# Kernel tuning notes

Measured on AMD Instinct MI355X. Metric: run time of the kernel, lower is better.

The kernel has to match this reference:

```python
import jax, jax.numpy as jnp
import numpy as np

S = 16          # spatial_size (adaptive pool output per dim)
EPS = 1e-8      # torch.cosine_similarity eps

def _avg_pool3d(x, s):
    # exact adaptive avg pool when D,H,W divisible by s
    B, C, D, H, W = x.shape
    kd, kh, kw = D // s, H // s, W // s
    x = x.reshape(B, C, s, kd, s, kh, s, kw)
    return x.mean(axis=(3, 5, 7))  # (B, C, s, s, s)

def _flatten_rows(x):
    # (B,C,s,s,s) -> (B*s^3, C), matching view+transpose+flatten
    B, C = x.shape[0], x.shape[1]
    return x.reshape(B, C, -1).transpose(0, 2, 1).reshape(-1, C)

def _cos_sim_matrix(a):
    # pairwise cosine similarity via normalize + GEMM
    norms = jnp.maximum(jnp.linalg.norm(a, axis=-1, keepdims=True), EPS)
    an = a / norms
    return an @ an.T  # (N, N)

def setup_inputs() -> dict:
    key = jax.random.key(0)
    k1, k2 = jax.random.split(key)
    shape = (2, 32, 64, 64, 64)
    p1 = jax.random.normal(k1, shape, dtype=jnp.float32)
    p2 = jax.random.normal(k2, shape, dtype=jnp.float32)
    return {"p1": p1, "p2": p2}

def reference(p1, p2):
    aa = _flatten_rows(_avg_pool3d(p1, S))  # (N, C), N = B*S^3
    bb = _flatten_rows(_avg_pool3d(p2, S))
    sim_a = _cos_sim_matrix(aa)
    sim_b = _cos_sim_matrix(bb)
    return jnp.mean((sim_a - sim_b) ** 2)  # MSELoss
```

## Files before the change

### kernel.cpp

```cpp
#include <hip/hip_runtime.h>
#include <hip/hip_bf16.h>


#define HW   4096
#define DHW  262144
#define NROW 8192
#define C    32

__global__ __launch_bounds__(256) void pool_norm_kernel(
    const float* __restrict__ p1, const float* __restrict__ p2,
    float* __restrict__ An, float* __restrict__ Bn)
{
    const int bid = blockIdx.x;
    const int y = bid & 15;
    const int z = (bid >> 4) & 15;
    const int b = bid >> 8;

    const float* __restrict__ src = (blockIdx.y == 0) ? p1 : p2;
    float* __restrict__ dst       = (blockIdx.y == 0) ? An : Bn;

    const int tid = threadIdx.x;
    const int x  = tid & 15;
    const int c0 = tid >> 4;

    __shared__ float pool[C][16];
    __shared__ float inv_norm[16];

    float pooled[2];
    #pragma unroll
    for (int cc = 0; cc < 2; ++cc) {
        const int c = c0 + cc * 16;
        const float* base = src + (size_t)(b * C + c) * DHW
                                + (4 * z) * HW + (4 * y) * 64 + 4 * x;
        float s = 0.f;
        #pragma unroll
        for (int dz = 0; dz < 4; ++dz) {
            #pragma unroll
            for (int dy = 0; dy < 4; ++dy) {
                const float4 v = *reinterpret_cast<const float4*>(base + dz * HW + dy * 64);
                s += (v.x + v.y) + (v.z + v.w);
            }
        }
        pooled[cc] = s * (1.0f / 64.0f);
        pool[c][x] = pooled[cc];
    }
    __syncthreads();

    if (tid < 16) {
        float ss = 0.f;
        #pragma unroll
        for (int c = 0; c < C; ++c) { const float v = pool[c][tid]; ss += v * v; }
        inv_norm[tid] = 1.0f / fmaxf(sqrtf(ss), 1e-8f);
    }
    __syncthreads();

    const int row = ((b * 16 + z) * 16 + y) * 16 + x;
    const float inv = inv_norm[x];
    #pragma unroll
    for (int cc = 0; cc < 2; ++cc) {
        const int c = c0 + cc * 16;
        dst[(size_t)row * C + c] = pooled[cc] * inv;
    }
}

__global__ __launch_bounds__(256) void gram_kernel(
    const float* __restrict__ An, const float* __restrict__ Bn,
    float* __restrict__ G)
{
    const int tid = threadIdx.x;
    const int k  = tid >> 3;
    const int l4 = (tid & 7) * 4;

    __shared__ float As[32 * C];
    __shared__ float Bs[32 * C];

    float gaa[4] = {0.f, 0.f, 0.f, 0.f};
    float gab[4] = {0.f, 0.f, 0.f, 0.f};
    float gbb[4] = {0.f, 0.f, 0.f, 0.f};

    const int row0 = blockIdx.x * 64;
    for (int t = 0; t < 2; ++t) {
        const int r = row0 + t * 32;
        reinterpret_cast<float4*>(As)[tid] =
            reinterpret_cast<const float4*>(An + (size_t)r * C)[tid];
        reinterpret_cast<float4*>(Bs)[tid] =
            reinterpret_cast<const float4*>(Bn + (size_t)r * C)[tid];
        __syncthreads();

        #pragma unroll
        for (int i = 0; i < 32; ++i) {
            const float a_k = As[i * C + k];
            const float b_k = Bs[i * C + k];
            const float4 a_l = *reinterpret_cast<const float4*>(&As[i * C + l4]);
            const float4 b_l = *reinterpret_cast<const float4*>(&Bs[i * C + l4]);
            gaa[0] += a_k * a_l.x;  gaa[1] += a_k * a_l.y;
            gaa[2] += a_k * a_l.z;  gaa[3] += a_k * a_l.w;
            gab[0] += a_k * b_l.x;  gab[1] += a_k * b_l.y;
            gab[2] += a_k * b_l.z;  gab[3] += a_k * b_l.w;
            gbb[0] += b_k * b_l.x;  gbb[1] += b_k * b_l.y;
            gbb[2] += b_k * b_l.z;  gbb[3] += b_k * b_l.w;
        }
        __syncthreads();
    }

    float* Gaa = G;
    float* Gab = G + 1024;
    float* Gbb = G + 2048;
    #pragma unroll
    for (int j = 0; j < 4; ++j) {
        atomicAdd(&Gaa[k * C + l4 + j], gaa[j]);
        atomicAdd(&Gab[k * C + l4 + j], gab[j]);
        atomicAdd(&Gbb[k * C + l4 + j], gbb[j]);
    }
}

__global__ __launch_bounds__(1024) void finalize_kernel(
    const float* __restrict__ G, float* __restrict__ out)
{
    const int t = threadIdx.x;
    const float gaa = G[t];
    const float gab = G[1024 + t];
    const float gbb = G[2048 + t];
    float v = gaa * gaa + gbb * gbb - 2.f * gab * gab;

    __shared__ float red[16];
    #pragma unroll
    for (int off = 32; off > 0; off >>= 1) v += __shfl_down(v, off);
    if ((t & 63) == 0) red[t >> 6] = v;
    __syncthreads();
    if (t < 16) {
        float w = red[t];
        #pragma unroll
        for (int off = 8; off > 0; off >>= 1) w += __shfl_down(w, off);
        if (t == 0) out[0] = w / ((float)NROW * (float)NROW);
    }
}

extern "C" void kernel_launch(void* const* d_in, const int* in_sizes, int n_in,
                              void* d_out, int out_size, void* d_ws, size_t ws_size,
                              hipStream_t stream) {
    const float* p1 = (const float*)d_in[0];
    const float* p2 = (const float*)d_in[1];
    float* out = (float*)d_out;

    float* An = (float*)d_ws;
    float* Bn = An + (size_t)NROW * C;
    float* G  = Bn + (size_t)NROW * C;

    hipMemsetAsync(G, 0, 3 * 1024 * sizeof(float), stream);

    dim3 g1(512, 2);
    pool_norm_kernel<<<g1, 256, 0, stream>>>(p1, p2, An, Bn);
    gram_kernel<<<128, 256, 0, stream>>>(An, Bn, G);
    finalize_kernel<<<1, 1024, 0, stream>>>(G, out);
}
```

Measured before the change: 162.6 us.

## Coalesce pooling loads across wave lanes and split gram atomics into partitions

The pooling kernel now runs 1024 threads per block. Each wave handles two channels, and its lanes cover the dy rows and x positions, so every float4 load is contiguous across lanes and all loads are issued before any summing. Partial sums are combined with wave shuffles. The gram kernel processes 32 rows per block across twice as many blocks, and it spreads its atomic adds over 8 partitioned copies of G to reduce contention; finalize then sums the partitions. The costs are a larger memset and the extra partition reads in finalize.

```diff
diff --git a/kernel.cpp b/kernel.cpp
--- a/kernel.cpp
+++ b/kernel.cpp
@@ -2,64 +2,69 @@
 #include <hip/hip_bf16.h>
 
 
-#define HW   4096
-#define DHW  262144
-#define NROW 8192
-#define C    32
+#define HW    4096
+#define DHW   262144
+#define NROW  8192
+#define C     32
+#define NPART 8
 
-__global__ __launch_bounds__(256) void pool_norm_kernel(
+__global__ __launch_bounds__(1024) void pool_norm_kernel(
     const float* __restrict__ p1, const float* __restrict__ p2,
     float* __restrict__ An, float* __restrict__ Bn)
 {
     const int bid = blockIdx.x;
-    const int y = bid & 15;
-    const int z = (bid >> 4) & 15;
-    const int b = bid >> 8;
+    const int yo = bid & 15;
+    const int zo = (bid >> 4) & 15;
+    const int b  = bid >> 8;
 
     const float* __restrict__ src = (blockIdx.y == 0) ? p1 : p2;
     float* __restrict__ dst       = (blockIdx.y == 0) ? An : Bn;
 
-    const int tid = threadIdx.x;
-    const int x  = tid & 15;
-    const int c0 = tid >> 4;
+    const int tid  = threadIdx.x;
+    const int wv   = tid >> 6;
+    const int lane = tid & 63;
+    const int dy   = lane >> 4;
+    const int x4   = lane & 15;
 
     __shared__ float pool[C][16];
     __shared__ float inv_norm[16];
 
-    float pooled[2];
+    float4 v[2][4];
     #pragma unroll
     for (int cc = 0; cc < 2; ++cc) {
-        const int c = c0 + cc * 16;
+        const int c = wv * 2 + cc;
         const float* base = src + (size_t)(b * C + c) * DHW
-                                + (4 * z) * HW + (4 * y) * 64 + 4 * x;
+                          + (4 * zo) * HW + (4 * yo + dy) * 64 + 4 * x4;
+        #pragma unroll
+        for (int dz = 0; dz < 4; ++dz)
+            v[cc][dz] = *reinterpret_cast<const float4*>(base + dz * HW);
+    }
+
+    #pragma unroll
+    for (int cc = 0; cc < 2; ++cc) {
         float s = 0.f;
         #pragma unroll
-        for (int dz = 0; dz < 4; ++dz) {
-            #pragma unroll
-            for (int dy = 0; dy < 4; ++dy) {
-                const float4 v = *reinterpret_cast<const float4*>(base + dz * HW + dy * 64);
-                s += (v.x + v.y) + (v.z + v.w);
-            }
-        }
-        pooled[cc] = s * (1.0f / 64.0f);
-        pool[c][x] = pooled[cc];
+        for (int dz = 0; dz < 4; ++dz)
+            s += (v[cc][dz].x + v[cc][dz].y) + (v[cc][dz].z + v[cc][dz].w);
+        s += __shfl_xor(s, 16);
+        s += __shfl_xor(s, 32);
+        if (lane < 16) pool[wv * 2 + cc][lane] = s * (1.0f / 64.0f);
     }
     __syncthreads();
 
     if (tid < 16) {
         float ss = 0.f;
         #pragma unroll
-        for (int c = 0; c < C; ++c) { const float v = pool[c][tid]; ss += v * v; }
+        for (int c = 0; c < C; ++c) { const float p = pool[c][tid]; ss += p * p; }
         inv_norm[tid] = 1.0f / fmaxf(sqrtf(ss), 1e-8f);
     }
     __syncthreads();
 
-    const int row = ((b * 16 + z) * 16 + y) * 16 + x;
-    const float inv = inv_norm[x];
-    #pragma unroll
-    for (int cc = 0; cc < 2; ++cc) {
-        const int c = c0 + cc * 16;
-        dst[(size_t)row * C + c] = pooled[cc] * inv;
+    if (tid < 512) {
+        const int x = tid >> 5;
+        const int c = tid & 31;
+        const int row = ((b * 16 + zo) * 16 + yo) * 16 + x;
+        dst[(size_t)row * C + c] = pool[c][x] * inv_norm[x];
     }
 }
 
@@ -78,39 +83,33 @@
     float gab[4] = {0.f, 0.f, 0.f, 0.f};
     float gbb[4] = {0.f, 0.f, 0.f, 0.f};
 
-    const int row0 = blockIdx.x * 64;
-    for (int t = 0; t < 2; ++t) {
-        const int r = row0 + t * 32;
-        reinterpret_cast<float4*>(As)[tid] =
-            reinterpret_cast<const float4*>(An + (size_t)r * C)[tid];
-        reinterpret_cast<float4*>(Bs)[tid] =
-            reinterpret_cast<const float4*>(Bn + (size_t)r * C)[tid];
-        __syncthreads();
+    const int r = blockIdx.x * 32;
+    reinterpret_cast<float4*>(As)[tid] =
+        reinterpret_cast<const float4*>(An + (size_t)r * C)[tid];
+    reinterpret_cast<float4*>(Bs)[tid] =
+        reinterpret_cast<const float4*>(Bn + (size_t)r * C)[tid];
+    __syncthreads();
 
-        #pragma unroll
-        for (int i = 0; i < 32; ++i) {
-            const float a_k = As[i * C + k];
-            const float b_k = Bs[i * C + k];
-            const float4 a_l = *reinterpret_cast<const float4*>(&As[i * C + l4]);
-            const float4 b_l = *reinterpret_cast<const float4*>(&Bs[i * C + l4]);
-            gaa[0] += a_k * a_l.x;  gaa[1] += a_k * a_l.y;
-            gaa[2] += a_k * a_l.z;  gaa[3] += a_k * a_l.w;
-            gab[0] += a_k * b_l.x;  gab[1] += a_k * b_l.y;
-            gab[2] += a_k * b_l.z;  gab[3] += a_k * b_l.w;
-            gbb[0] += b_k * b_l.x;  gbb[1] += b_k * b_l.y;
-            gbb[2] += b_k * b_l.z;  gbb[3] += b_k * b_l.w;
-        }
-        __syncthreads();
+    #pragma unroll
+    for (int i = 0; i < 32; ++i) {
+        const float a_k = As[i * C + k];
+        const float b_k = Bs[i * C + k];
+        const float4 a_l = *reinterpret_cast<const float4*>(&As[i * C + l4]);
+        const float4 b_l = *reinterpret_cast<const float4*>(&Bs[i * C + l4]);
+        gaa[0] += a_k * a_l.x;  gaa[1] += a_k * a_l.y;
+        gaa[2] += a_k * a_l.z;  gaa[3] += a_k * a_l.w;
+        gab[0] += a_k * b_l.x;  gab[1] += a_k * b_l.y;
+        gab[2] += a_k * b_l.z;  gab[3] += a_k * b_l.w;
+        gbb[0] += b_k * b_l.x;  gbb[1] += b_k * b_l.y;
+        gbb[2] += b_k * b_l.z;  gbb[3] += b_k * b_l.w;
     }
 
-    float* Gaa = G;
-    float* Gab = G + 1024;
-    float* Gbb = G + 2048;
+    float* Gp = G + (size_t)(blockIdx.x & (NPART - 1)) * 3072;
     #pragma unroll
     for (int j = 0; j < 4; ++j) {
-        atomicAdd(&Gaa[k * C + l4 + j], gaa[j]);
-        atomicAdd(&Gab[k * C + l4 + j], gab[j]);
-        atomicAdd(&Gbb[k * C + l4 + j], gbb[j]);
+        atomicAdd(&Gp[k * C + l4 + j],        gaa[j]);
+        atomicAdd(&Gp[1024 + k * C + l4 + j], gab[j]);
+        atomicAdd(&Gp[2048 + k * C + l4 + j], gbb[j]);
     }
 }
 
@@ -118,9 +117,13 @@
     const float* __restrict__ G, float* __restrict__ out)
 {
     const int t = threadIdx.x;
-    const float gaa = G[t];
-    const float gab = G[1024 + t];
-    const float gbb = G[2048 + t];
+    float gaa = 0.f, gab = 0.f, gbb = 0.f;
+    #pragma unroll
+    for (int p = 0; p < NPART; ++p) {
+        gaa += G[p * 3072 + t];
+        gab += G[p * 3072 + 1024 + t];
+        gbb += G[p * 3072 + 2048 + t];
+    }
     float v = gaa * gaa + gbb * gbb - 2.f * gab * gab;
 
     __shared__ float red[16];
@@ -147,10 +150,10 @@
     float* Bn = An + (size_t)NROW * C;
     float* G  = Bn + (size_t)NROW * C;
 
-    hipMemsetAsync(G, 0, 3 * 1024 * sizeof(float), stream);
+    hipMemsetAsync(G, 0, NPART * 3072 * sizeof(float), stream);
 
     dim3 g1(512, 2);
-    pool_norm_kernel<<<g1, 256, 0, stream>>>(p1, p2, An, Bn);
-    gram_kernel<<<128, 256, 0, stream>>>(An, Bn, G);
+    pool_norm_kernel<<<g1, 1024, 0, stream>>>(p1, p2, An, Bn);
+    gram_kernel<<<256, 256, 0, stream>>>(An, Bn, G);
     finalize_kernel<<<1, 1024, 0, stream>>>(G, out);
 }
```

Result: no change. 160.7 us (-1.1%).
